# Performance work log

Hardware: AMD Instinct MI355X
Metric: run time of the kernel (lower is better)

The kernel has to match this reference:

```python
import jax, jax.numpy as jnp
import numpy as np

B, M, H, D, K, V = 32, 4096, 32, 4096, 128, 128

def setup_inputs() -> dict:
    key = jax.random.key(0)
    ks = jax.random.split(key, 7)
    s = lambda fan: 1.0 / np.sqrt(fan)
    return {
        "x": jax.random.normal(ks[0], (B, D), jnp.float32),
        "K_prev": jax.random.normal(ks[1], (B, M, K), jnp.float32),
        "V_prev": jax.random.normal(ks[2], (B, M, V), jnp.float32),
        "P_q": jax.random.normal(ks[3], (H, D, K), jnp.float32) * s(D),
        "P_k": jax.random.normal(ks[4], (D, K), jnp.float32) * s(D),
        "P_v": jax.random.normal(ks[5], (D, V), jnp.float32) * s(D),
        "P_o": jax.random.normal(ks[6], (H, D, V), jnp.float32) * s(D),
    }

def reference(x, K_prev, V_prev, P_q, P_k, P_v, P_o):
    # per-head query projection: [b,d] x [h,d,k] -> [b,h,k]
    q = jnp.einsum('bd,hdk->bhk', x, P_q)
    # shared (multi-query) K/V projection of the new token, appended to cache
    k_new = jnp.einsum('bd,dk->bk', x, P_k)          # [b,k]
    v_new = jnp.einsum('bd,dv->bv', x, P_v)          # [b,v]
    K_new = jnp.concatenate([K_prev, k_new[:, None, :]], axis=1)  # [b,m+1,k]
    V_new = jnp.concatenate([V_prev, v_new[:, None, :]], axis=1)  # [b,m+1,v]
    # attention over shared cache
    logits = jnp.einsum('bhk,bmk->bhm', q, K_new)    # [b,h,m+1]
    w = jax.nn.softmax(logits, axis=-1)
    o = jnp.einsum('bhm,bmv->bhv', w, V_new)         # [b,h,v]
    y = jnp.einsum('bhv,hdv->bd', o, P_o)            # [b,d]
    return (y, K_new, V_new)
```

## Files before the change

kernel.cpp:

```cpp
#include <hip/hip_runtime.h>

#define B_ 32
#define M_ 4096
#define M1_ 4097
#define H_ 32
#define D_ 4096

typedef float float4_ __attribute__((ext_vector_type(4)));
typedef float f32x4 __attribute__((ext_vector_type(4)));
typedef short short8 __attribute__((ext_vector_type(8)));

#define KOFF 131072
#define VOFF 16912384
#define QPART_OFF 0u
#define Q_OFF     2228224u
#define APART_OFF 2367488u
#define O_OFF     6692864u
#define YPART_OFF 6823936u

__device__ __forceinline__ unsigned short f2bf(float f) {
  union { float f; unsigned u; } cv; cv.f = f;
  return (unsigned short)((cv.u + 0x7FFFu + ((cv.u >> 16) & 1u)) >> 16);
}

__device__ __forceinline__ short8 pack8(const float* t) {
  short8 r;
#pragma unroll
  for (int j = 0; j < 8; ++j) r[j] = (short)f2bf(t[j]);
  return r;
}

__device__ __forceinline__ short8 load8cvt(const float* __restrict__ p) {
  float t[8];
  float4_ v0 = *(const float4_*)p;
  float4_ v1 = *(const float4_*)(p + 4);
#pragma unroll
  for (int j = 0; j < 4; ++j) { t[j] = v0[j]; t[4 + j] = v1[j]; }
  return pack8(t);
}

__global__ __launch_bounds__(256) void k_proj(const float* __restrict__ x,
    const float* __restrict__ Pq, const float* __restrict__ Pk,
    const float* __restrict__ Pv, float* __restrict__ qpart)
{
  int bid = blockIdx.x;
  int hh = bid >> 4;
  int c  = bid & 15;
  const float* W = (hh < 32) ? (Pq + (size_t)hh * D_ * 128)
                             : ((hh == 32) ? Pk : Pv);
  int d0 = c * 256;
  int tid = threadIdx.x;
  int w = tid >> 6, l = tid & 63, l15 = l & 15, lg = l >> 4;
  f32x4 acc[2][2] = {};
  for (int ks = 0; ks < 8; ++ks) {
    int dk = d0 + ks * 32 + lg * 8;
    short8 af[2];
#pragma unroll
    for (int bt = 0; bt < 2; ++bt)
      af[bt] = load8cvt(x + (size_t)(bt * 16 + l15) * D_ + dk);
    short8 bf[2];
#pragma unroll
    for (int nti = 0; nti < 2; ++nti) {
      int col = (2 * w + nti) * 16 + l15;
      float t[8];
#pragma unroll
      for (int j = 0; j < 8; ++j) t[j] = W[(size_t)(dk + j) * 128 + col];
      bf[nti] = pack8(t);
    }
#pragma unroll
    for (int bt = 0; bt < 2; ++bt)
#pragma unroll
      for (int nti = 0; nti < 2; ++nti)
        acc[bt][nti] = __builtin_amdgcn_mfma_f32_16x16x32_bf16(af[bt], bf[nti], acc[bt][nti], 0, 0, 0);
  }
#pragma unroll
  for (int bt = 0; bt < 2; ++bt)
#pragma unroll
    for (int nti = 0; nti < 2; ++nti) {
      int k = (2 * w + nti) * 16 + l15;
#pragma unroll
      for (int i = 0; i < 4; ++i) {
        int b = bt * 16 + lg * 4 + i;
        qpart[(size_t)((c * 34 + hh) * 32 + b) * 128 + k] = acc[bt][nti][i];
      }
    }
}

__global__ __launch_bounds__(256) void k_reduce_q(const float* __restrict__ qpart,
    float* __restrict__ q, float* __restrict__ dout)
{
  int idx = blockIdx.x * 256 + threadIdx.x;
  if (idx >= 34 * 32 * 128) return;
  float s = 0.f;
#pragma unroll
  for (int cc = 0; cc < 16; ++cc) s += qpart[(size_t)cc * 139264 + idx];
  q[idx] = s;
  int hh = idx >> 12;
  if (hh >= 32) {
    int b = (idx >> 7) & 31, k = idx & 127;
    size_t off = (hh == 32) ? (size_t)KOFF : (size_t)VOFF;
    dout[off + ((size_t)b * M1_ + M_) * 128 + k] = s;
  }
}

__global__ __launch_bounds__(256) void k_attn(const float* __restrict__ Kp,
    const float* __restrict__ Vp, const float* __restrict__ q,
    float* __restrict__ dout, float* __restrict__ apart)
{
  __shared__ float S[32][136];
  __shared__ unsigned short P[32][128];
  __shared__ float smax[32], ssum[32], sextra[32];
  int bid = blockIdx.x;
  int b = bid >> 5, c = bid & 31;
  int m0 = c * 128;
  int tid = threadIdx.x, w = tid >> 6, l = tid & 63, l15 = l & 15, lg = l >> 4;
  const float* Kt = Kp + ((size_t)b * M_ + m0) * 128;
  const float* Vt = Vp + ((size_t)b * M_ + m0) * 128;
  float* Kn = dout + KOFF + ((size_t)b * M1_ + m0) * 128;
  float* Vn = dout + VOFF + ((size_t)b * M1_ + m0) * 128;

#pragma unroll
  for (int i = 0; i < 16; ++i) {
    int idx = tid + i * 256;
    ((float4_*)Kn)[idx] = ((const float4_*)Kt)[idx];
  }

  f32x4 sacc[2][2] = {};
#pragma unroll
  for (int ks = 0; ks < 4; ++ks) {
    short8 af[2], bf[2];
#pragma unroll
    for (int ht = 0; ht < 2; ++ht) {
      int h = ht * 16 + l15;
      af[ht] = load8cvt(q + (size_t)(h * 32 + b) * 128 + ks * 32 + lg * 8);
    }
#pragma unroll
    for (int mti = 0; mti < 2; ++mti) {
      int m = (2 * w + mti) * 16 + l15;
      bf[mti] = load8cvt(Kt + (size_t)m * 128 + ks * 32 + lg * 8);
    }
#pragma unroll
    for (int ht = 0; ht < 2; ++ht)
#pragma unroll
      for (int mti = 0; mti < 2; ++mti)
        sacc[ht][mti] = __builtin_amdgcn_mfma_f32_16x16x32_bf16(af[ht], bf[mti], sacc[ht][mti], 0, 0, 0);
  }
#pragma unroll
  for (int ht = 0; ht < 2; ++ht)
#pragma unroll
    for (int mti = 0; mti < 2; ++mti)
#pragma unroll
      for (int i = 0; i < 4; ++i)
        S[ht * 16 + lg * 4 + i][(2 * w + mti) * 16 + l15] = sacc[ht][mti][i];

  if (c == 31 && tid < 32) {
    int h = tid;
    const float* qh = q + (size_t)(h * 32 + b) * 128;
    const float* kn = q + (size_t)(32 * 32 + b) * 128;
    float s = 0.f;
    for (int k = 0; k < 128; ++k) s += qh[k] * kn[k];
    S[h][128] = s;
  }
  __syncthreads();

  {
    int h = tid >> 3, i = tid & 7;
    float vals[16];
    float mx = -1e30f;
#pragma unroll
    for (int j = 0; j < 16; ++j) { vals[j] = S[h][i * 16 + j]; mx = fmaxf(mx, vals[j]); }
#pragma unroll
    for (int d = 1; d < 8; d <<= 1) mx = fmaxf(mx, __shfl_xor(mx, d));
    if (c == 31) mx = fmaxf(mx, S[h][128]);
    float se = 0.f;
#pragma unroll
    for (int j = 0; j < 16; ++j) {
      float p = __expf(vals[j] - mx);
      se += p;
      P[h][(i * 16 + j) ^ ((h & 7) << 3)] = f2bf(p);
    }
    if (c == 31 && i == 0) { float pe = __expf(S[h][128] - mx); se += pe; sextra[h] = pe; }
#pragma unroll
    for (int d = 1; d < 8; d <<= 1) se += __shfl_xor(se, d);
    if (i == 0) { smax[h] = mx; ssum[h] = se; }
  }
  __syncthreads();

#pragma unroll
  for (int i = 0; i < 16; ++i) {
    int idx = tid + i * 256;
    ((float4_*)Vn)[idx] = ((const float4_*)Vt)[idx];
  }

  f32x4 oacc[2][2] = {};
#pragma unroll
  for (int ks = 0; ks < 4; ++ks) {
    short8 af[2], bf[2];
#pragma unroll
    for (int ht = 0; ht < 2; ++ht) {
      int h = ht * 16 + l15;
      int mb = (ks * 32 + lg * 8) ^ ((h & 7) << 3);
      af[ht] = *(const short8*)&P[h][mb];
    }
#pragma unroll
    for (int vti = 0; vti < 2; ++vti) {
      int v = (2 * w + vti) * 16 + l15;
      float t[8];
#pragma unroll
      for (int j = 0; j < 8; ++j) t[j] = Vt[(size_t)(ks * 32 + lg * 8 + j) * 128 + v];
      bf[vti] = pack8(t);
    }
#pragma unroll
    for (int ht = 0; ht < 2; ++ht)
#pragma unroll
      for (int vti = 0; vti < 2; ++vti)
        oacc[ht][vti] = __builtin_amdgcn_mfma_f32_16x16x32_bf16(af[ht], bf[vti], oacc[ht][vti], 0, 0, 0);
  }

  const float* vnew = q + (size_t)(33 * 32 + b) * 128;
#pragma unroll
  for (int ht = 0; ht < 2; ++ht)
#pragma unroll
    for (int vti = 0; vti < 2; ++vti) {
      int v = (2 * w + vti) * 16 + l15;
#pragma unroll
      for (int i = 0; i < 4; ++i) {
        int h = ht * 16 + lg * 4 + i;
        float val = oacc[ht][vti][i];
        if (c == 31) val += sextra[h] * vnew[v];
        apart[((size_t)((b * 32 + c) * 32 + h)) * 132 + v] = val;
      }
    }
  if (tid < 32) {
    apart[((size_t)((b * 32 + c) * 32 + tid)) * 132 + 128] = smax[tid];
    apart[((size_t)((b * 32 + c) * 32 + tid)) * 132 + 129] = ssum[tid];
  }
}

__global__ void k_combine(const float* __restrict__ apart, float* __restrict__ o)
{
  int bid = blockIdx.x;
  int b = bid >> 5, h = bid & 31;
  int v = threadIdx.x;
  const float* base = apart + ((size_t)(b * 32) * 32 + h) * 132;
  float gm = -1e30f;
  for (int cc = 0; cc < 32; ++cc) gm = fmaxf(gm, base[(size_t)cc * 32 * 132 + 128]);
  float num = 0.f, den = 0.f;
  for (int cc = 0; cc < 32; ++cc) {
    const float* pc = base + (size_t)cc * 32 * 132;
    float sc = __expf(pc[128] - gm);
    num += sc * pc[v];
    den += sc * pc[129];
  }
  o[((size_t)(b * 32 + h)) * 128 + v] = num / den;
}

__global__ __launch_bounds__(256) void k_out(const float* __restrict__ o,
    const float* __restrict__ Po, float* __restrict__ ypart)
{
  int bid = blockIdx.x;
  int dt = bid >> 3, hg = bid & 7;
  int tid = threadIdx.x, w = tid >> 6, l = tid & 63, l15 = l & 15, lg = l >> 4;
  f32x4 acc[2][2] = {};
  for (int hi = 0; hi < 4; ++hi) {
    int h = hg * 4 + hi;
#pragma unroll
    for (int ks = 0; ks < 4; ++ks) {
      short8 af[2], bf[2];
#pragma unroll
      for (int bt = 0; bt < 2; ++bt)
        af[bt] = load8cvt(o + ((size_t)((bt * 16 + l15) * 32 + h)) * 128 + ks * 32 + lg * 8);
#pragma unroll
      for (int dtl = 0; dtl < 2; ++dtl) {
        int d = dt * 128 + (2 * w + dtl) * 16 + l15;
        bf[dtl] = load8cvt(Po + ((size_t)h * D_ + d) * 128 + ks * 32 + lg * 8);
      }
#pragma unroll
      for (int bt = 0; bt < 2; ++bt)
#pragma unroll
        for (int dtl = 0; dtl < 2; ++dtl)
          acc[bt][dtl] = __builtin_amdgcn_mfma_f32_16x16x32_bf16(af[bt], bf[dtl], acc[bt][dtl], 0, 0, 0);
    }
  }
#pragma unroll
  for (int bt = 0; bt < 2; ++bt)
#pragma unroll
    for (int dtl = 0; dtl < 2; ++dtl) {
      int d = dt * 128 + (2 * w + dtl) * 16 + l15;
#pragma unroll
      for (int i = 0; i < 4; ++i) {
        int b = bt * 16 + lg * 4 + i;
        ypart[((size_t)(hg * 32 + b)) * 4096 + d] = acc[bt][dtl][i];
      }
    }
}

__global__ __launch_bounds__(256) void k_reduce_y(const float* __restrict__ ypart,
    float* __restrict__ dout)
{
  int idx = blockIdx.x * 256 + threadIdx.x;
  float s = 0.f;
#pragma unroll
  for (int g = 0; g < 8; ++g) s += ypart[(size_t)g * 131072 + idx];
  dout[idx] = s;
}

extern "C" void kernel_launch(void* const* d_in, const int* in_sizes, int n_in,
                              void* d_out, int out_size, void* d_ws, size_t ws_size,
                              hipStream_t stream) {
  (void)in_sizes; (void)n_in; (void)out_size; (void)ws_size;
  const float* x  = (const float*)d_in[0];
  const float* Kp = (const float*)d_in[1];
  const float* Vp = (const float*)d_in[2];
  const float* Pq = (const float*)d_in[3];
  const float* Pk = (const float*)d_in[4];
  const float* Pv = (const float*)d_in[5];
  const float* Po = (const float*)d_in[6];
  float* out = (float*)d_out;
  float* ws  = (float*)d_ws;
  float* qpart = ws + QPART_OFF;
  float* q     = ws + Q_OFF;
  float* apart = ws + APART_OFF;
  float* o     = ws + O_OFF;
  float* ypart = ws + YPART_OFF;

  hipLaunchKernelGGL(k_proj,     dim3(544),  dim3(256), 0, stream, x, Pq, Pk, Pv, qpart);
  hipLaunchKernelGGL(k_reduce_q, dim3(544),  dim3(256), 0, stream, qpart, q, out);
  hipLaunchKernelGGL(k_attn,     dim3(1024), dim3(256), 0, stream, Kp, Vp, q, out, apart);
  hipLaunchKernelGGL(k_combine,  dim3(1024), dim3(128), 0, stream, apart, o);
  hipLaunchKernelGGL(k_out,      dim3(256),  dim3(256), 0, stream, o, Po, ypart);
  hipLaunchKernelGGL(k_reduce_y, dim3(512),  dim3(256), 0, stream, ypart, out);
}
```

Measured before the change: 140.1 us.

## Stage weights and V through LDS, halve attention chunk, store partials in bf16

k_proj now loads each 32-row weight slice with coalesced float4 reads, converts it to bf16 in LDS, and reads the strided B operand from shared memory. k_attn splits the cache into 64-row chunks across twice as many blocks. It loads K and V once into registers, uses them for both the cache copy and an LDS V tile, and writes per-chunk partial outputs as bf16 with max/sum stored separately. The aim is to remove uncoalesced strided global reads and the duplicate V fetch, and to shrink partial traffic, at the cost of more combine work, extra bf16 rounding of the partials, and more LDS and register pressure.

```diff
diff --git a/kernel.cpp b/kernel.cpp
--- a/kernel.cpp
+++ b/kernel.cpp
@@ -9,27 +9,32 @@
 typedef float float4_ __attribute__((ext_vector_type(4)));
 typedef float f32x4 __attribute__((ext_vector_type(4)));
 typedef short short8 __attribute__((ext_vector_type(8)));
+typedef short short4_ __attribute__((ext_vector_type(4)));
 
 #define KOFF 131072
 #define VOFF 16912384
-#define QPART_OFF 0u
-#define Q_OFF     2228224u
-#define APART_OFF 2367488u
-#define O_OFF     6692864u
-#define YPART_OFF 6823936u
+
+#define Q_OFF     0u
+#define O_OFF     139264u
+#define YPART_OFF 270336u
+#define QPART_OFF 1318912u
+#define APO_OFF   1318912u
+#define MSUM_OFF  5513216u
 
 __device__ __forceinline__ unsigned short f2bf(float f) {
   union { float f; unsigned u; } cv; cv.f = f;
   return (unsigned short)((cv.u + 0x7FFFu + ((cv.u >> 16) & 1u)) >> 16);
 }
-
+__device__ __forceinline__ float bf2f(unsigned short b) {
+  union { unsigned u; float f; } cv; cv.u = ((unsigned)b) << 16;
+  return cv.f;
+}
 __device__ __forceinline__ short8 pack8(const float* t) {
   short8 r;
 #pragma unroll
   for (int j = 0; j < 8; ++j) r[j] = (short)f2bf(t[j]);
   return r;
 }
-
 __device__ __forceinline__ short8 load8cvt(const float* __restrict__ p) {
   float t[8];
   float4_ v0 = *(const float4_*)p;
@@ -39,10 +44,11 @@
   return pack8(t);
 }
 
-__global__ __launch_bounds__(256) void k_proj(const float* __restrict__ x,
+__global__ __launch_bounds__(256, 4) void k_proj(const float* __restrict__ x,
     const float* __restrict__ Pq, const float* __restrict__ Pk,
     const float* __restrict__ Pv, float* __restrict__ qpart)
 {
+  __shared__ unsigned short Wl[2][32][128];
   int bid = blockIdx.x;
   int hh = bid >> 4;
   int c  = bid & 15;
@@ -53,6 +59,18 @@
   int w = tid >> 6, l = tid & 63, l15 = l & 15, lg = l >> 4;
   f32x4 acc[2][2] = {};
   for (int ks = 0; ks < 8; ++ks) {
+    int buf = ks & 1;
+#pragma unroll
+    for (int i = 0; i < 4; ++i) {
+      int idx = i * 256 + tid;
+      int dr = idx >> 5, k4 = (idx & 31) * 4;
+      float4_ t = *(const float4_*)(W + (size_t)(d0 + ks * 32 + dr) * 128 + k4);
+      short4_ s;
+#pragma unroll
+      for (int j = 0; j < 4; ++j) s[j] = (short)f2bf(t[j]);
+      *(short4_*)&Wl[buf][dr][k4] = s;
+    }
+    __syncthreads();
     int dk = d0 + ks * 32 + lg * 8;
     short8 af[2];
 #pragma unroll
@@ -62,10 +80,10 @@
 #pragma unroll
     for (int nti = 0; nti < 2; ++nti) {
       int col = (2 * w + nti) * 16 + l15;
-      float t[8];
-#pragma unroll
-      for (int j = 0; j < 8; ++j) t[j] = W[(size_t)(dk + j) * 128 + col];
-      bf[nti] = pack8(t);
+      short8 t;
+#pragma unroll
+      for (int j = 0; j < 8; ++j) t[j] = (short)Wl[buf][lg * 8 + j][col];
+      bf[nti] = t;
     }
 #pragma unroll
     for (int bt = 0; bt < 2; ++bt)
@@ -103,112 +121,110 @@
   }
 }
 
-__global__ __launch_bounds__(256) void k_attn(const float* __restrict__ Kp,
+__global__ __launch_bounds__(256, 4) void k_attn(const float* __restrict__ Kp,
     const float* __restrict__ Vp, const float* __restrict__ q,
-    float* __restrict__ dout, float* __restrict__ apart)
-{
-  __shared__ float S[32][136];
-  __shared__ unsigned short P[32][128];
+    float* __restrict__ dout, unsigned short* __restrict__ apo,
+    float* __restrict__ msum)
+{
+  __shared__ unsigned short Vl[64][128];
+  __shared__ float S[32][73];
+  __shared__ unsigned short P[32][64];
   __shared__ float smax[32], ssum[32], sextra[32];
   int bid = blockIdx.x;
-  int b = bid >> 5, c = bid & 31;
-  int m0 = c * 128;
+  int b = bid >> 6, c = bid & 63;
+  int m0 = c * 64;
   int tid = threadIdx.x, w = tid >> 6, l = tid & 63, l15 = l & 15, lg = l >> 4;
   const float* Kt = Kp + ((size_t)b * M_ + m0) * 128;
   const float* Vt = Vp + ((size_t)b * M_ + m0) * 128;
   float* Kn = dout + KOFF + ((size_t)b * M1_ + m0) * 128;
   float* Vn = dout + VOFF + ((size_t)b * M1_ + m0) * 128;
 
-#pragma unroll
-  for (int i = 0; i < 16; ++i) {
+  float4_ kr[8], vr[8];
+#pragma unroll
+  for (int i = 0; i < 8; ++i) kr[i] = ((const float4_*)Kt)[tid + i * 256];
+#pragma unroll
+  for (int i = 0; i < 8; ++i) vr[i] = ((const float4_*)Vt)[tid + i * 256];
+#pragma unroll
+  for (int i = 0; i < 8; ++i) ((float4_*)Kn)[tid + i * 256] = kr[i];
+#pragma unroll
+  for (int i = 0; i < 8; ++i) {
     int idx = tid + i * 256;
-    ((float4_*)Kn)[idx] = ((const float4_*)Kt)[idx];
-  }
-
-  f32x4 sacc[2][2] = {};
+    ((float4_*)Vn)[idx] = vr[i];
+    int m = idx >> 5, v = (idx & 31) * 4;
+    short4_ s;
+#pragma unroll
+    for (int j = 0; j < 4; ++j) s[j] = (short)f2bf(vr[i][j]);
+    *(short4_*)&Vl[m][v] = s;
+  }
+
+  f32x4 sacc[2] = {};
 #pragma unroll
   for (int ks = 0; ks < 4; ++ks) {
-    short8 af[2], bf[2];
+    short8 bfK = load8cvt(Kt + (size_t)(w * 16 + l15) * 128 + ks * 32 + lg * 8);
 #pragma unroll
     for (int ht = 0; ht < 2; ++ht) {
-      int h = ht * 16 + l15;
-      af[ht] = load8cvt(q + (size_t)(h * 32 + b) * 128 + ks * 32 + lg * 8);
-    }
-#pragma unroll
-    for (int mti = 0; mti < 2; ++mti) {
-      int m = (2 * w + mti) * 16 + l15;
-      bf[mti] = load8cvt(Kt + (size_t)m * 128 + ks * 32 + lg * 8);
-    }
-#pragma unroll
-    for (int ht = 0; ht < 2; ++ht)
-#pragma unroll
-      for (int mti = 0; mti < 2; ++mti)
-        sacc[ht][mti] = __builtin_amdgcn_mfma_f32_16x16x32_bf16(af[ht], bf[mti], sacc[ht][mti], 0, 0, 0);
+      short8 af = load8cvt(q + (size_t)((ht * 16 + l15) * 32 + b) * 128 + ks * 32 + lg * 8);
+      sacc[ht] = __builtin_amdgcn_mfma_f32_16x16x32_bf16(af, bfK, sacc[ht], 0, 0, 0);
+    }
   }
 #pragma unroll
   for (int ht = 0; ht < 2; ++ht)
 #pragma unroll
-    for (int mti = 0; mti < 2; ++mti)
-#pragma unroll
-      for (int i = 0; i < 4; ++i)
-        S[ht * 16 + lg * 4 + i][(2 * w + mti) * 16 + l15] = sacc[ht][mti][i];
-
-  if (c == 31 && tid < 32) {
+    for (int i = 0; i < 4; ++i)
+      S[ht * 16 + lg * 4 + i][w * 16 + l15] = sacc[ht][i];
+
+  if (c == 63 && tid < 32) {
     int h = tid;
     const float* qh = q + (size_t)(h * 32 + b) * 128;
     const float* kn = q + (size_t)(32 * 32 + b) * 128;
     float s = 0.f;
     for (int k = 0; k < 128; ++k) s += qh[k] * kn[k];
-    S[h][128] = s;
+    S[h][64] = s;
   }
   __syncthreads();
 
   {
     int h = tid >> 3, i = tid & 7;
-    float vals[16];
-    float mx = -1e30f;
-#pragma unroll
-    for (int j = 0; j < 16; ++j) { vals[j] = S[h][i * 16 + j]; mx = fmaxf(mx, vals[j]); }
+    float vals[8];
+    float mx = -3e38f;
+#pragma unroll
+    for (int j = 0; j < 8; ++j) { vals[j] = S[h][i * 8 + j]; mx = fmaxf(mx, vals[j]); }
 #pragma unroll
     for (int d = 1; d < 8; d <<= 1) mx = fmaxf(mx, __shfl_xor(mx, d));
-    if (c == 31) mx = fmaxf(mx, S[h][128]);
+    if (c == 63) mx = fmaxf(mx, S[h][64]);
     float se = 0.f;
-#pragma unroll
-    for (int j = 0; j < 16; ++j) {
+    short8 pw;
+#pragma unroll
+    for (int j = 0; j < 8; ++j) {
       float p = __expf(vals[j] - mx);
       se += p;
-      P[h][(i * 16 + j) ^ ((h & 7) << 3)] = f2bf(p);
-    }
-    if (c == 31 && i == 0) { float pe = __expf(S[h][128] - mx); se += pe; sextra[h] = pe; }
+      pw[j] = (short)f2bf(p);
+    }
+    *(short8*)((char*)P + h * 128 + ((i * 16) ^ ((h & 7) << 4))) = pw;
+    if (c == 63 && i == 0) { float pe = __expf(S[h][64] - mx); se += pe; sextra[h] = pe; }
 #pragma unroll
     for (int d = 1; d < 8; d <<= 1) se += __shfl_xor(se, d);
     if (i == 0) { smax[h] = mx; ssum[h] = se; }
   }
   __syncthreads();
 
-#pragma unroll
-  for (int i = 0; i < 16; ++i) {
-    int idx = tid + i * 256;
-    ((float4_*)Vn)[idx] = ((const float4_*)Vt)[idx];
-  }
-
   f32x4 oacc[2][2] = {};
 #pragma unroll
-  for (int ks = 0; ks < 4; ++ks) {
-    short8 af[2], bf[2];
+  for (int ksv = 0; ksv < 2; ++ksv) {
+    short8 af[2];
 #pragma unroll
     for (int ht = 0; ht < 2; ++ht) {
       int h = ht * 16 + l15;
-      int mb = (ks * 32 + lg * 8) ^ ((h & 7) << 3);
-      af[ht] = *(const short8*)&P[h][mb];
-    }
+      af[ht] = *(const short8*)((const char*)P + h * 128 + ((ksv * 64 + lg * 16) ^ ((h & 7) << 4)));
+    }
+    short8 bf[2];
 #pragma unroll
     for (int vti = 0; vti < 2; ++vti) {
-      int v = (2 * w + vti) * 16 + l15;
-      float t[8];
-#pragma unroll
-      for (int j = 0; j < 8; ++j) t[j] = Vt[(size_t)(ks * 32 + lg * 8 + j) * 128 + v];
-      bf[vti] = pack8(t);
+      int v = w * 32 + vti * 16 + l15;
+      short8 t;
+#pragma unroll
+      for (int j = 0; j < 8; ++j) t[j] = (short)Vl[ksv * 32 + lg * 8 + j][v];
+      bf[vti] = t;
     }
 #pragma unroll
     for (int ht = 0; ht < 2; ++ht)
@@ -222,35 +238,37 @@
   for (int ht = 0; ht < 2; ++ht)
 #pragma unroll
     for (int vti = 0; vti < 2; ++vti) {
-      int v = (2 * w + vti) * 16 + l15;
+      int v = w * 32 + vti * 16 + l15;
 #pragma unroll
       for (int i = 0; i < 4; ++i) {
         int h = ht * 16 + lg * 4 + i;
         float val = oacc[ht][vti][i];
-        if (c == 31) val += sextra[h] * vnew[v];
-        apart[((size_t)((b * 32 + c) * 32 + h)) * 132 + v] = val;
+        if (c == 63) val += sextra[h] * vnew[v];
+        apo[((size_t)(b * 64 + c) * 32 + h) * 128 + v] = f2bf(val);
       }
     }
   if (tid < 32) {
-    apart[((size_t)((b * 32 + c) * 32 + tid)) * 132 + 128] = smax[tid];
-    apart[((size_t)((b * 32 + c) * 32 + tid)) * 132 + 129] = ssum[tid];
-  }
-}
-
-__global__ void k_combine(const float* __restrict__ apart, float* __restrict__ o)
+    size_t base = ((size_t)(b * 64 + c) * 32 + tid) * 2;
+    msum[base]     = smax[tid];
+    msum[base + 1] = ssum[tid];
+  }
+}
+
+__global__ void k_combine(const unsigned short* __restrict__ apo,
+    const float* __restrict__ msum, float* __restrict__ o)
 {
   int bid = blockIdx.x;
   int b = bid >> 5, h = bid & 31;
   int v = threadIdx.x;
-  const float* base = apart + ((size_t)(b * 32) * 32 + h) * 132;
-  float gm = -1e30f;
-  for (int cc = 0; cc < 32; ++cc) gm = fmaxf(gm, base[(size_t)cc * 32 * 132 + 128]);
+  float gm = -3e38f;
+  for (int cc = 0; cc < 64; ++cc)
+    gm = fmaxf(gm, msum[((size_t)(b * 64 + cc) * 32 + h) * 2]);
   float num = 0.f, den = 0.f;
-  for (int cc = 0; cc < 32; ++cc) {
-    const float* pc = base + (size_t)cc * 32 * 132;
-    float sc = __expf(pc[128] - gm);
-    num += sc * pc[v];
-    den += sc * pc[129];
+  for (int cc = 0; cc < 64; ++cc) {
+    size_t slot = (size_t)(b * 64 + cc) * 32 + h;
+    float sc = __expf(msum[slot * 2] - gm);
+    num += sc * bf2f(apo[slot * 128 + v]);
+    den += sc * msum[slot * 2 + 1];
   }
   o[((size_t)(b * 32 + h)) * 128 + v] = num / den;
 }
@@ -318,16 +336,17 @@
   const float* Po = (const float*)d_in[6];
   float* out = (float*)d_out;
   float* ws  = (float*)d_ws;
-  float* qpart = ws + QPART_OFF;
   float* q     = ws + Q_OFF;
-  float* apart = ws + APART_OFF;
   float* o     = ws + O_OFF;
   float* ypart = ws + YPART_OFF;
+  float* qpart = ws + QPART_OFF;
+  unsigned short* apo = (unsigned short*)(ws + APO_OFF);
+  float* msum  = ws + MSUM_OFF;
 
   hipLaunchKernelGGL(k_proj,     dim3(544),  dim3(256), 0, stream, x, Pq, Pk, Pv, qpart);
   hipLaunchKernelGGL(k_reduce_q, dim3(544),  dim3(256), 0, stream, qpart, q, out);
-  hipLaunchKernelGGL(k_attn,     dim3(1024), dim3(256), 0, stream, Kp, Vp, q, out, apart);
-  hipLaunchKernelGGL(k_combine,  dim3(1024), dim3(128), 0, stream, apart, o);
+  hipLaunchKernelGGL(k_attn,     dim3(2048), dim3(256), 0, stream, Kp, Vp, q, out, apo, msum);
+  hipLaunchKernelGGL(k_combine,  dim3(1024), dim3(128), 0, stream, apo, msum, o);
   hipLaunchKernelGGL(k_out,      dim3(256),  dim3(256), 0, stream, o, Po, ypart);
   hipLaunchKernelGGL(k_reduce_y, dim3(512),  dim3(256), 0, stream, ypart, out);
 }
```

New measurement: 149.6 us. 6.8% more time.
